# Performance work log

Hardware: AMD Instinct MI355X
Metric: run time of the kernel (lower is better)

Reference implementation:

```python
import jax, jax.numpy as jnp
import numpy as np

DIM = 1024
HEADS = 16
HEAD_DIM = DIM // HEADS
DFF = 4 * DIM
EPS = 1e-6


def _layernorm(x, scale, bias):
    mu = jnp.mean(x, axis=-1, keepdims=True)
    var = jnp.mean(jnp.square(x - mu), axis=-1, keepdims=True)
    return (x - mu) * jax.lax.rsqrt(var + EPS) * scale + bias


def setup_inputs() -> dict:
    key = jax.random.key(0)
    ks = jax.random.split(key, 8)
    d = {}
    d["x"] = jax.random.normal(ks[0], (4, 2048, DIM), dtype=jnp.float32)
    # LayerNorm params
    d["ln1_scale"] = jnp.ones((DIM,), jnp.float32)
    d["ln1_bias"] = jnp.zeros((DIM,), jnp.float32)
    d["ln2_scale"] = jnp.ones((DIM,), jnp.float32)
    d["ln2_bias"] = jnp.zeros((DIM,), jnp.float32)
    # Attention params
    d["qkv_w"] = jax.random.normal(ks[1], (DIM, 3 * DIM), jnp.float32) * (DIM ** -0.5)
    d["qkv_b"] = jnp.zeros((3 * DIM,), jnp.float32)
    d["proj_w"] = jax.random.normal(ks[2], (DIM, DIM), jnp.float32) * (DIM ** -0.5)
    d["proj_b"] = jnp.zeros((DIM,), jnp.float32)
    # MLP params
    d["fc1_w"] = jax.random.normal(ks[3], (DIM, DFF), jnp.float32) * (DIM ** -0.5)
    d["fc1_b"] = jnp.zeros((DFF,), jnp.float32)
    d["fc2_w"] = jax.random.normal(ks[4], (DFF, DIM), jnp.float32) * (DFF ** -0.5)
    d["fc2_b"] = jnp.zeros((DIM,), jnp.float32)
    return d


def reference(x, ln1_scale, ln1_bias, ln2_scale, ln2_bias,
              qkv_w, qkv_b, proj_w, proj_b,
              fc1_w, fc1_b, fc2_w, fc2_b):
    B, S, D = x.shape
    scale = HEAD_DIM ** -0.5

    # --- Attention sub-block (pre-LN) ---
    h = _layernorm(x, ln1_scale, ln1_bias)
    qkv = h @ qkv_w + qkv_b                                  # [B,S,3D]
    qkv = qkv.reshape(B, S, 3, HEADS, HEAD_DIM)
    qkv = qkv.transpose(2, 0, 3, 1, 4)                       # [3,B,H,S,hd]
    q, k, v = qkv[0], qkv[1], qkv[2]
    attn = jnp.einsum('bhqd,bhkd->bhqk', q, k) * scale       # [B,H,S,S]
    attn = jax.nn.softmax(attn, axis=-1)
    out = jnp.einsum('bhqk,bhkd->bhqd', attn, v)             # [B,H,S,hd]
    out = out.transpose(0, 2, 1, 3).reshape(B, S, D)
    out = out @ proj_w + proj_b
    x = x + out

    # --- MLP sub-block (pre-LN) ---
    h = _layernorm(x, ln2_scale, ln2_bias)
    h = jax.nn.gelu(h @ fc1_w + fc1_b)
    h = h @ fc2_w + fc2_b
    return x + h
```

## Files before the change

### kernel.cpp

```cpp
#include <hip/hip_runtime.h>
#include <hip/hip_bf16.h>

typedef __attribute__((ext_vector_type(4))) float f32x4;
typedef __attribute__((ext_vector_type(16))) float f32x16;
typedef __attribute__((ext_vector_type(8))) short bf16x8;

__device__ __forceinline__ unsigned short f2bf(float f) {
    return __bfloat16_as_ushort(__float2bfloat16(f));
}

typedef __attribute__((address_space(1))) const unsigned char* gas_ptr;
typedef __attribute__((address_space(3))) unsigned char* las_ptr;
__device__ __forceinline__ void gload16(const void* g, void* l) {
    __builtin_amdgcn_global_load_lds((gas_ptr)g, (las_ptr)l, 16, 0, 0);
}

__device__ __forceinline__ unsigned cvt_pk_bf16(float lo, float hi) {
    unsigned r;
    asm("v_cvt_pk_bf16_f32 %0, %1, %2" : "=v"(r) : "v"(lo), "v"(hi));
    return r;
}

__device__ __forceinline__ void plswap(unsigned &a, unsigned &b) {
    unsigned sa = (unsigned)__shfl_xor((int)a, 32);
    unsigned sb = (unsigned)__shfl_xor((int)b, 32);
    bool lo = (threadIdx.x & 63) < 32;
    unsigned na = lo ? sb : a;
    unsigned nb = lo ? b : sa;
    a = na; b = nb;
}

__global__ __launch_bounds__(256) void ln_kernel(
    const float* __restrict__ x, const float* __restrict__ scale,
    const float* __restrict__ bias, unsigned short* __restrict__ out)
{
    int row = blockIdx.x;
    const float* xr = x + (size_t)row * 1024;
    int t = threadIdx.x;
    float4 v = ((const float4*)xr)[t];
    float s  = v.x + v.y + v.z + v.w;
    float ss = v.x*v.x + v.y*v.y + v.z*v.z + v.w*v.w;
    #pragma unroll
    for (int m = 32; m; m >>= 1) { s += __shfl_down(s, m); ss += __shfl_down(ss, m); }
    __shared__ float red[8];
    int wid = t >> 6;
    if ((t & 63) == 0) { red[wid*2] = s; red[wid*2+1] = ss; }
    __syncthreads();
    s  = red[0] + red[2] + red[4] + red[6];
    ss = red[1] + red[3] + red[5] + red[7];
    float mu  = s * (1.0f/1024.0f);
    float var = ss * (1.0f/1024.0f) - mu*mu;
    float inv = rsqrtf(var + 1e-6f);
    float4 sc = ((const float4*)scale)[t];
    float4 bi = ((const float4*)bias)[t];
    ushort4 o;
    o.x = f2bf((v.x - mu)*inv*sc.x + bi.x);
    o.y = f2bf((v.y - mu)*inv*sc.y + bi.y);
    o.z = f2bf((v.z - mu)*inv*sc.z + bi.z);
    o.w = f2bf((v.w - mu)*inv*sc.w + bi.w);
    ((ushort4*)(out + (size_t)row * 1024))[t] = o;
}

__global__ __launch_bounds__(256) void transpose_kernel(
    const float* __restrict__ W, unsigned short* __restrict__ Wt, int K, int N)
{
    __shared__ float tile[32][33];
    int n0 = blockIdx.x * 32, k0 = blockIdx.y * 32;
    int tx = threadIdx.x, ty = threadIdx.y;
    #pragma unroll
    for (int j = 0; j < 32; j += 8)
        tile[ty + j][tx] = W[(size_t)(k0 + ty + j) * N + n0 + tx];
    __syncthreads();
    #pragma unroll
    for (int j = 0; j < 32; j += 8)
        Wt[(size_t)(n0 + ty + j) * K + k0 + tx] = f2bf(tile[tx][ty + j]);
}

template<int EPI>
__global__ __launch_bounds__(256) void gemm_kernel(
    const unsigned short* __restrict__ A,
    const unsigned short* __restrict__ Bt,
    const float* __restrict__ bias,
    const float* __restrict__ res,
    void* __restrict__ out,
    unsigned short* __restrict__ vtout,
    int M, int N, int K)
{
    __shared__ unsigned short Al[128 * 64];
    __shared__ unsigned short Bl[128 * 64];
    int t = threadIdx.x;
    int wid = t >> 6, lane = t & 63;
    int wr = wid >> 1, wc = wid & 1;
    int l15 = lane & 15, lg = lane >> 4;
    int brow = blockIdx.y * 128, bcol = blockIdx.x * 128;
    f32x4 acc[4][4] = {};
    int srow = t >> 3;
    int scol = (t & 7) * 8;
    const unsigned short* ga = A  + (size_t)(brow + srow) * K + scol;
    const unsigned short* gb = Bt + (size_t)(bcol + srow) * K + scol;
    char* la = (char*)Al + wid * 1024;
    char* lb = (char*)Bl + wid * 1024;

    for (int k0 = 0; k0 < K; k0 += 64) {
        __syncthreads();
        #pragma unroll
        for (int i = 0; i < 4; i++) {
            gload16(ga + k0 + (size_t)(i * 32) * K, la + i * 4096);
            gload16(gb + k0 + (size_t)(i * 32) * K, lb + i * 4096);
        }
        __syncthreads();
        #pragma unroll
        for (int kf = 0; kf < 2; kf++) {
            bf16x8 af[4], bfr[4];
            #pragma unroll
            for (int m = 0; m < 4; m++) af[m]  = *(const bf16x8*)&Al[(wr*64 + m*16 + l15)*64 + kf*32 + lg*8];
            #pragma unroll
            for (int n = 0; n < 4; n++) bfr[n] = *(const bf16x8*)&Bl[(wc*64 + n*16 + l15)*64 + kf*32 + lg*8];
            #pragma unroll
            for (int m = 0; m < 4; m++)
                #pragma unroll
                for (int n = 0; n < 4; n++)
                    acc[m][n] = __builtin_amdgcn_mfma_f32_16x16x32_bf16(af[m], bfr[n], acc[m][n], 0, 0, 0);
        }
    }

    #pragma unroll
    for (int m = 0; m < 4; m++) {
        #pragma unroll
        for (int n = 0; n < 4; n++) {
            int col = bcol + wc*64 + n*16 + l15;
            float bs = bias[col];
            #pragma unroll
            for (int r = 0; r < 4; r++) {
                int row = brow + wr*64 + m*16 + lg*4 + r;
                size_t idx = (size_t)row * N + col;
                float v = acc[m][n][r] + bs;
                if (EPI == 1) {
                    ((float*)out)[idx] = v + res[idx];
                } else if (EPI == 2) {
                    float u = v + 0.044715f * v * v * v;
                    float e = __builtin_amdgcn_exp2f(-2.3022077f * u);
                    float g = v * __builtin_amdgcn_rcpf(1.0f + e);
                    ((unsigned short*)out)[idx] = f2bf(g);
                } else {
                    unsigned short bv = f2bf(v);
                    ((unsigned short*)out)[idx] = bv;
                    if (col >= 2048) {
                        int hd = col - 2048;
                        int b = row >> 11, s = row & 2047;
                        vtout[((size_t)((b << 4) + (hd >> 6)) * 64 + (hd & 63)) * 2048 + s] = bv;
                    }
                }
            }
        }
    }
}

__global__ __launch_bounds__(512, 2) void attn_kernel(
    const unsigned short* __restrict__ qkv, const unsigned short* __restrict__ vt,
    unsigned short* __restrict__ ctx)
{
    __shared__ unsigned short Kl[2][4096];
    __shared__ unsigned short Vl[2][4096];

    int t = threadIdx.x;
    int wid = t >> 6, lane = t & 63;
    int l31 = lane & 31, half = lane >> 5;
    int bh = blockIdx.y;
    int b = bh >> 4, h = bh & 15;
    int qr0 = blockIdx.x * 256 + wid * 32;

    const size_t qbase = (size_t)b * 2048 * 3072 + (size_t)h * 64;
    const unsigned short* vbase = vt + (size_t)bh * 64 * 2048;

    bf16x8 qf[4];
    #pragma unroll
    for (int ds = 0; ds < 4; ds++)
        qf[ds] = *(const bf16x8*)(qkv + qbase + (size_t)(qr0 + l31) * 3072 + ds*16 + half*8);

    f32x16 ot0 = {}, ot1 = {};
    float mrun = -1e30f, lrun = 0.0f;
    const float C = 0.125f * 1.44269504f;

    int srow = t >> 3;
    int ssw = ((t & 7) * 16) ^ ((srow & 7) << 4);
    const unsigned short* kg = qkv + qbase + 1024 + (size_t)srow * 3072 + (ssw >> 1);
    const unsigned short* vg = vbase + (size_t)srow * 2048 + (ssw >> 1);

    gload16(kg, (char*)Kl[0] + t * 16);
    gload16(vg, (char*)Vl[0] + t * 16);
    __syncthreads();

    int cur = 0;
    for (int kt = 0; kt < 32; kt++) {
        if (kt < 31) {
            gload16(kg + (size_t)(kt + 1) * 64 * 3072, (char*)Kl[cur ^ 1] + t * 16);
            gload16(vg + (kt + 1) * 64,               (char*)Vl[cur ^ 1] + t * 16);
        }

        const char* Kb = (const char*)Kl[cur];
        const char* Vb = (const char*)Vl[cur];

        f32x16 st0 = {}, st1 = {};
        __builtin_amdgcn_s_setprio(1);
        #pragma unroll
        for (int ds = 0; ds < 4; ds++) {
            int colb = ds*32 + half*16;
            int sw = (l31 & 7) << 4;
            bf16x8 k0 = *(const bf16x8*)(Kb + l31*128 + (colb ^ sw));
            bf16x8 k1 = *(const bf16x8*)(Kb + (32 + l31)*128 + (colb ^ sw));
            st0 = __builtin_amdgcn_mfma_f32_32x32x16_bf16(k0, qf[ds], st0, 0, 0, 0);
            st1 = __builtin_amdgcn_mfma_f32_32x32x16_bf16(k1, qf[ds], st1, 0, 0, 0);
        }
        __builtin_amdgcn_s_setprio(0);

        float mx = fmaxf(st0[0], st0[1]);
        #pragma unroll
        for (int r = 2; r < 16; r++) mx = fmaxf(mx, st0[r]);
        #pragma unroll
        for (int r = 0; r < 16; r++) mx = fmaxf(mx, st1[r]);
        mx = fmaxf(mx, __shfl_xor(mx, 32));
        float pm = mx * C;

        bool grow = pm > mrun + 11.5416f;
        if (__any(grow)) {
            float mn = fmaxf(mrun, pm);
            float corr = __builtin_amdgcn_exp2f(mrun - mn);
            mrun = mn;
            lrun *= corr;
            ot0 *= corr;
            ot1 *= corr;
        }

        unsigned w0[8], w1[8];
        float sum = 0.0f;
        {
            float e[16];
            #pragma unroll
            for (int r = 0; r < 16; r++) { e[r] = __builtin_amdgcn_exp2f(fmaf(st0[r], C, -mrun)); sum += e[r]; }
            #pragma unroll
            for (int p = 0; p < 8; p++) w0[p] = cvt_pk_bf16(e[2*p], e[2*p+1]);
            #pragma unroll
            for (int r = 0; r < 16; r++) { e[r] = __builtin_amdgcn_exp2f(fmaf(st1[r], C, -mrun)); sum += e[r]; }
            #pragma unroll
            for (int p = 0; p < 8; p++) w1[p] = cvt_pk_bf16(e[2*p], e[2*p+1]);
        }
        lrun += sum;
        plswap(w0[2], w0[0]); plswap(w0[3], w0[1]);
        plswap(w0[6], w0[4]); plswap(w0[7], w0[5]);
        plswap(w1[2], w1[0]); plswap(w1[3], w1[1]);
        plswap(w1[6], w1[4]); plswap(w1[7], w1[5]);

        __builtin_amdgcn_s_setprio(1);
        #pragma unroll
        for (int ks = 0; ks < 4; ks++) {
            union { unsigned u[4]; bf16x8 v; } pf;
            unsigned* w = (ks < 2) ? w0 : w1;
            int o4 = (ks & 1) * 4;
            pf.u[0] = w[o4 + 0]; pf.u[1] = w[o4 + 1]; pf.u[2] = w[o4 + 2]; pf.u[3] = w[o4 + 3];
            int colb = ks*32 + half*16;
            int sw = (l31 & 7) << 4;
            bf16x8 v0 = *(const bf16x8*)(Vb + l31*128 + (colb ^ sw));
            bf16x8 v1 = *(const bf16x8*)(Vb + (32 + l31)*128 + (colb ^ sw));
            ot0 = __builtin_amdgcn_mfma_f32_32x32x16_bf16(v0, pf.v, ot0, 0, 0, 0);
            ot1 = __builtin_amdgcn_mfma_f32_32x32x16_bf16(v1, pf.v, ot1, 0, 0, 0);
        }
        __builtin_amdgcn_s_setprio(0);

        __syncthreads();
        cur ^= 1;
    }

    float ltot = lrun + __shfl_xor(lrun, 32);
    float rl = 1.0f / ltot;
    size_t cb = (size_t)b * 2048 * 1024 + (size_t)(qr0 + l31) * 1024 + (size_t)h * 64;
    #pragma unroll
    for (int r = 0; r < 16; r++) {
        int d = (r & 3) + 8 * (r >> 2) + 4 * half;
        ctx[cb + d]      = f2bf(ot0[r] * rl);
        ctx[cb + 32 + d] = f2bf(ot1[r] * rl);
    }
}

extern "C" void kernel_launch(void* const* d_in, const int* in_sizes, int n_in,
                              void* d_out, int out_size, void* d_ws, size_t ws_size,
                              hipStream_t stream) {
    const float* x      = (const float*)d_in[0];
    const float* ln1_s  = (const float*)d_in[1];
    const float* ln1_b  = (const float*)d_in[2];
    const float* ln2_s  = (const float*)d_in[3];
    const float* ln2_b  = (const float*)d_in[4];
    const float* qkv_w  = (const float*)d_in[5];
    const float* qkv_b  = (const float*)d_in[6];
    const float* proj_w = (const float*)d_in[7];
    const float* proj_b = (const float*)d_in[8];
    const float* fc1_w  = (const float*)d_in[9];
    const float* fc1_b  = (const float*)d_in[10];
    const float* fc2_w  = (const float*)d_in[11];
    const float* fc2_b  = (const float*)d_in[12];
    float* out = (float*)d_out;

    char* ws = (char*)d_ws;
    unsigned short* vtb  = (unsigned short*)(ws + 0);
    float*          x1   = (float*)(ws + 0);
    unsigned short* h    = (unsigned short*)(ws + (size_t)32 * 1024 * 1024);
    unsigned short* qkvb = (unsigned short*)(ws + (size_t)48 * 1024 * 1024);
    unsigned short* gbuf = (unsigned short*)(ws + (size_t)48 * 1024 * 1024);
    unsigned short* ctxb = (unsigned short*)(ws + (size_t)96 * 1024 * 1024);
    unsigned short* wT   = (unsigned short*)(ws + (size_t)112 * 1024 * 1024);

    dim3 tb(32, 8);

    transpose_kernel<<<dim3(96, 32), tb, 0, stream>>>(qkv_w, wT, 1024, 3072);
    ln_kernel<<<8192, 256, 0, stream>>>(x, ln1_s, ln1_b, h);
    gemm_kernel<3><<<dim3(24, 64), 256, 0, stream>>>(h, wT, qkv_b, nullptr, qkvb, vtb, 8192, 3072, 1024);
    attn_kernel<<<dim3(8, 64), 512, 0, stream>>>(qkvb, vtb, ctxb);
    transpose_kernel<<<dim3(32, 32), tb, 0, stream>>>(proj_w, wT, 1024, 1024);
    gemm_kernel<1><<<dim3(8, 64), 256, 0, stream>>>(ctxb, wT, proj_b, x, x1, nullptr, 8192, 1024, 1024);
    ln_kernel<<<8192, 256, 0, stream>>>(x1, ln2_s, ln2_b, h);
    transpose_kernel<<<dim3(128, 32), tb, 0, stream>>>(fc1_w, wT, 1024, 4096);
    gemm_kernel<2><<<dim3(32, 64), 256, 0, stream>>>(h, wT, fc1_b, nullptr, gbuf, nullptr, 8192, 4096, 1024);
    transpose_kernel<<<dim3(32, 128), tb, 0, stream>>>(fc2_w, wT, 4096, 1024);
    gemm_kernel<1><<<dim3(8, 64), 256, 0, stream>>>(gbuf, wT, fc2_b, x1, out, nullptr, 8192, 1024, 4096);
}
```

Measured before the change: 471.5 us.

## Double-buffer LDS tiles in GEMM to overlap global loads with MFMA

Gives the GEMM kernel two LDS buffers for the A and B tiles and issues the global-to-LDS loads for the next K tile before computing on the current one, keeping one barrier per iteration instead of two. The aim is to hide global memory latency behind MFMA work. It doubles LDS use to 64KB per block, which may lower occupancy. The prefetch relies on the end-of-iteration barrier to cover completion of the async direct-to-LDS loads, which may not be enough without an explicit vmcnt wait.

```diff
diff --git a/kernel.cpp b/kernel.cpp
--- a/kernel.cpp
+++ b/kernel.cpp
@@ -86,8 +86,8 @@
     unsigned short* __restrict__ vtout,
     int M, int N, int K)
 {
-    __shared__ unsigned short Al[128 * 64];
-    __shared__ unsigned short Bl[128 * 64];
+    __shared__ unsigned short Al[2][128 * 64];
+    __shared__ unsigned short Bl[2][128 * 64];
     int t = threadIdx.x;
     int wid = t >> 6, lane = t & 63;
     int wr = wid >> 1, wc = wid & 1;
@@ -98,30 +98,47 @@
     int scol = (t & 7) * 8;
     const unsigned short* ga = A  + (size_t)(brow + srow) * K + scol;
     const unsigned short* gb = Bt + (size_t)(bcol + srow) * K + scol;
-    char* la = (char*)Al + wid * 1024;
-    char* lb = (char*)Bl + wid * 1024;
-
-    for (int k0 = 0; k0 < K; k0 += 64) {
-        __syncthreads();
+
+    {
+        char* la = (char*)Al[0] + wid * 1024;
+        char* lb = (char*)Bl[0] + wid * 1024;
         #pragma unroll
         for (int i = 0; i < 4; i++) {
-            gload16(ga + k0 + (size_t)(i * 32) * K, la + i * 4096);
-            gload16(gb + k0 + (size_t)(i * 32) * K, lb + i * 4096);
-        }
-        __syncthreads();
+            gload16(ga + (size_t)(i * 32) * K, la + i * 4096);
+            gload16(gb + (size_t)(i * 32) * K, lb + i * 4096);
+        }
+    }
+    __syncthreads();
+
+    int nk = K >> 6;
+    for (int kt = 0; kt < nk; kt++) {
+        int cur = kt & 1;
+        if (kt + 1 < nk) {
+            char* la = (char*)Al[cur ^ 1] + wid * 1024;
+            char* lb = (char*)Bl[cur ^ 1] + wid * 1024;
+            int k1 = (kt + 1) << 6;
+            #pragma unroll
+            for (int i = 0; i < 4; i++) {
+                gload16(ga + k1 + (size_t)(i * 32) * K, la + i * 4096);
+                gload16(gb + k1 + (size_t)(i * 32) * K, lb + i * 4096);
+            }
+        }
+        const unsigned short* Ab = Al[cur];
+        const unsigned short* Bb = Bl[cur];
         #pragma unroll
         for (int kf = 0; kf < 2; kf++) {
             bf16x8 af[4], bfr[4];
             #pragma unroll
-            for (int m = 0; m < 4; m++) af[m]  = *(const bf16x8*)&Al[(wr*64 + m*16 + l15)*64 + kf*32 + lg*8];
-            #pragma unroll
-            for (int n = 0; n < 4; n++) bfr[n] = *(const bf16x8*)&Bl[(wc*64 + n*16 + l15)*64 + kf*32 + lg*8];
+            for (int m = 0; m < 4; m++) af[m]  = *(const bf16x8*)&Ab[(wr*64 + m*16 + l15)*64 + kf*32 + lg*8];
+            #pragma unroll
+            for (int n = 0; n < 4; n++) bfr[n] = *(const bf16x8*)&Bb[(wc*64 + n*16 + l15)*64 + kf*32 + lg*8];
             #pragma unroll
             for (int m = 0; m < 4; m++)
                 #pragma unroll
                 for (int n = 0; n < 4; n++)
                     acc[m][n] = __builtin_amdgcn_mfma_f32_16x16x32_bf16(af[m], bfr[n], acc[m][n], 0, 0, 0);
         }
+        __syncthreads();
     }
 
     #pragma unroll
```

Result: no change. 466.1 us (-1.1%).

## Replace GEMM with 256-row double-buffered swizzled-LDS kernel and XCD tile remap

Applied to the files above, without the earlier changes.

Replaces the 128x128 single-buffered GEMM with a 256xBN tile kernel using 512 threads, double-buffered LDS staging that overlaps the next K-tile load with MFMA work, XOR-swizzled LDS addressing to avoid bank conflicts, and a workgroup index remap that groups neighbouring tiles on the same XCD. It also raises MFMA priority around the compute blocks. The aim is more data reuse per tile and hidden global-load latency in all four projection GEMMs. In exchange, LDS use and register pressure per block go up, and there are fewer blocks to fill the chip.

```diff
diff --git a/kernel.cpp b/kernel.cpp
--- a/kernel.cpp
+++ b/kernel.cpp
@@ -76,8 +76,8 @@
         Wt[(size_t)(n0 + ty + j) * K + k0 + tx] = f2bf(tile[tx][ty + j]);
 }
 
-template<int EPI>
-__global__ __launch_bounds__(256) void gemm_kernel(
+template<int EPI, int BN>
+__global__ __launch_bounds__(512, 2) void gemm256_kernel(
     const unsigned short* __restrict__ A,
     const unsigned short* __restrict__ Bt,
     const float* __restrict__ bias,
@@ -86,55 +86,108 @@
     unsigned short* __restrict__ vtout,
     int M, int N, int K)
 {
-    __shared__ unsigned short Al[128 * 64];
-    __shared__ unsigned short Bl[128 * 64];
+    constexpr int BM = 256;
+    constexpr int WARPS_N = (BN == 256) ? 4 : 2;
+    constexpr int WM = (BN == 256) ? 128 : 64;
+    constexpr int WN = 64;
+    constexpr int MQ = WM / 64;
+    constexpr int NF = WN / 16;
+    constexpr int NB = BN / 64;
+
+    __shared__ __align__(16) unsigned short Al[2][BM * 64];
+    __shared__ __align__(16) unsigned short Bl[2][BN * 64];
+
     int t = threadIdx.x;
     int wid = t >> 6, lane = t & 63;
-    int wr = wid >> 1, wc = wid & 1;
+    int wr = wid / WARPS_N, wc = wid % WARPS_N;
     int l15 = lane & 15, lg = lane >> 4;
-    int brow = blockIdx.y * 128, bcol = blockIdx.x * 128;
-    f32x4 acc[4][4] = {};
-    int srow = t >> 3;
-    int scol = (t & 7) * 8;
-    const unsigned short* ga = A  + (size_t)(brow + srow) * K + scol;
-    const unsigned short* gb = Bt + (size_t)(bcol + srow) * K + scol;
-    char* la = (char*)Al + wid * 1024;
-    char* lb = (char*)Bl + wid * 1024;
-
-    for (int k0 = 0; k0 < K; k0 += 64) {
-        __syncthreads();
-        #pragma unroll
-        for (int i = 0; i < 4; i++) {
-            gload16(ga + k0 + (size_t)(i * 32) * K, la + i * 4096);
-            gload16(gb + k0 + (size_t)(i * 32) * K, lb + i * 4096);
-        }
-        __syncthreads();
-        #pragma unroll
-        for (int kf = 0; kf < 2; kf++) {
-            bf16x8 af[4], bfr[4];
-            #pragma unroll
-            for (int m = 0; m < 4; m++) af[m]  = *(const bf16x8*)&Al[(wr*64 + m*16 + l15)*64 + kf*32 + lg*8];
-            #pragma unroll
-            for (int n = 0; n < 4; n++) bfr[n] = *(const bf16x8*)&Bl[(wc*64 + n*16 + l15)*64 + kf*32 + lg*8];
-            #pragma unroll
-            for (int m = 0; m < 4; m++)
+
+    int gx = gridDim.x;
+    int nwg = gx * gridDim.y;
+    int orig = blockIdx.y * gx + blockIdx.x;
+    int cpx = nwg >> 3;
+    int wg = (orig & 7) * cpx + (orig >> 3);
+    int bx = wg % gx, by = wg / gx;
+    int brow = by * BM, bcol = bx * BN;
+
+    f32x4 acc[MQ * 4][NF] = {};
+
+    int sr  = t >> 3;
+    int scb = (t & 7) * 16;
+    int sce = (scb ^ ((sr & 7) << 4)) >> 1;
+    const size_t aoff = (size_t)(brow + sr) * K + sce;
+    const size_t boff = (size_t)(bcol + sr) * K + sce;
+
+    auto stage = [&](int b, int kt2) {
+        int k0 = kt2 << 6;
+        char* la = (char*)Al[b] + (wid << 10);
+        char* lb = (char*)Bl[b] + (wid << 10);
+        #pragma unroll
+        for (int i = 0; i < 4; i++)
+            gload16(A + aoff + (size_t)(i * 64) * K + k0, la + i * 8192);
+        #pragma unroll
+        for (int j = 0; j < NB; j++)
+            gload16(Bt + boff + (size_t)(j * 64) * K + k0, lb + j * 8192);
+    };
+
+    stage(0, 0);
+    asm volatile("s_waitcnt vmcnt(0)" ::: "memory");
+    __builtin_amdgcn_s_barrier();
+
+    int nk = K >> 6;
+    int rsw = (l15 & 7) << 4;
+    for (int kt = 0; kt < nk; kt++) {
+        int cur = kt & 1;
+        if (kt + 1 < nk) stage(cur ^ 1, kt + 1);
+
+        const char* Ab = (const char*)Al[cur];
+        const char* Bb = (const char*)Bl[cur];
+
+        bf16x8 bfr[NF][2];
+        #pragma unroll
+        for (int nf = 0; nf < NF; nf++) {
+            int rb = wc * WN + nf * 16 + l15;
+            #pragma unroll
+            for (int kk = 0; kk < 2; kk++)
+                bfr[nf][kk] = *(const bf16x8*)(Bb + rb * 128 + ((kk * 64 + lg * 16) ^ rsw));
+        }
+        #pragma unroll
+        for (int mq = 0; mq < MQ; mq++) {
+            bf16x8 af[4][2];
+            #pragma unroll
+            for (int mf = 0; mf < 4; mf++) {
+                int ra = wr * WM + mq * 64 + mf * 16 + l15;
                 #pragma unroll
-                for (int n = 0; n < 4; n++)
-                    acc[m][n] = __builtin_amdgcn_mfma_f32_16x16x32_bf16(af[m], bfr[n], acc[m][n], 0, 0, 0);
-        }
+                for (int kk = 0; kk < 2; kk++)
+                    af[mf][kk] = *(const bf16x8*)(Ab + ra * 128 + ((kk * 64 + lg * 16) ^ rsw));
+            }
+            __builtin_amdgcn_s_setprio(1);
+            #pragma unroll
+            for (int mf = 0; mf < 4; mf++)
+                #pragma unroll
+                for (int nf = 0; nf < NF; nf++)
+                    #pragma unroll
+                    for (int kk = 0; kk < 2; kk++)
+                        acc[mq*4+mf][nf] = __builtin_amdgcn_mfma_f32_16x16x32_bf16(
+                            af[mf][kk], bfr[nf][kk], acc[mq*4+mf][nf], 0, 0, 0);
+            __builtin_amdgcn_s_setprio(0);
+        }
+
+        asm volatile("s_waitcnt vmcnt(0)" ::: "memory");
+        __builtin_amdgcn_s_barrier();
     }
 
     #pragma unroll
-    for (int m = 0; m < 4; m++) {
-        #pragma unroll
-        for (int n = 0; n < 4; n++) {
-            int col = bcol + wc*64 + n*16 + l15;
+    for (int mi = 0; mi < MQ * 4; mi++) {
+        #pragma unroll
+        for (int nf = 0; nf < NF; nf++) {
+            int col = bcol + wc * WN + nf * 16 + l15;
             float bs = bias[col];
             #pragma unroll
             for (int r = 0; r < 4; r++) {
-                int row = brow + wr*64 + m*16 + lg*4 + r;
+                int row = brow + wr * WM + mi * 16 + lg * 4 + r;
                 size_t idx = (size_t)row * N + col;
-                float v = acc[m][n][r] + bs;
+                float v = acc[mi][nf][r] + bs;
                 if (EPI == 1) {
                     ((float*)out)[idx] = v + res[idx];
                 } else if (EPI == 2) {
@@ -313,13 +366,13 @@
 
     transpose_kernel<<<dim3(96, 32), tb, 0, stream>>>(qkv_w, wT, 1024, 3072);
     ln_kernel<<<8192, 256, 0, stream>>>(x, ln1_s, ln1_b, h);
-    gemm_kernel<3><<<dim3(24, 64), 256, 0, stream>>>(h, wT, qkv_b, nullptr, qkvb, vtb, 8192, 3072, 1024);
+    gemm256_kernel<3,128><<<dim3(24, 32), 512, 0, stream>>>(h, wT, qkv_b, nullptr, qkvb, vtb, 8192, 3072, 1024);
     attn_kernel<<<dim3(8, 64), 512, 0, stream>>>(qkvb, vtb, ctxb);
     transpose_kernel<<<dim3(32, 32), tb, 0, stream>>>(proj_w, wT, 1024, 1024);
-    gemm_kernel<1><<<dim3(8, 64), 256, 0, stream>>>(ctxb, wT, proj_b, x, x1, nullptr, 8192, 1024, 1024);
+    gemm256_kernel<1,128><<<dim3(8, 32), 512, 0, stream>>>(ctxb, wT, proj_b, x, x1, nullptr, 8192, 1024, 1024);
     ln_kernel<<<8192, 256, 0, stream>>>(x1, ln2_s, ln2_b, h);
     transpose_kernel<<<dim3(128, 32), tb, 0, stream>>>(fc1_w, wT, 1024, 4096);
-    gemm_kernel<2><<<dim3(32, 64), 256, 0, stream>>>(h, wT, fc1_b, nullptr, gbuf, nullptr, 8192, 4096, 1024);
+    gemm256_kernel<2,256><<<dim3(16, 32), 512, 0, stream>>>(h, wT, fc1_b, nullptr, gbuf, nullptr, 8192, 4096, 1024);
     transpose_kernel<<<dim3(32, 128), tb, 0, stream>>>(fc2_w, wT, 4096, 1024);
-    gemm_kernel<1><<<dim3(8, 64), 256, 0, stream>>>(gbuf, wT, fc2_b, x1, out, nullptr, 8192, 1024, 4096);
-}
+    gemm256_kernel<1,128><<<dim3(8, 32), 512, 0, stream>>>(gbuf, wT, fc2_b, x1, out, nullptr, 8192, 1024, 4096);
+}
```

New measurement: 426.7 us. 1.1x faster.
